# Optimization experiments

Hardware: AMD Instinct MI355X
Metric: run time of the kernel (lower is better)

The kernel has to match this reference:

```python
import jax, jax.numpy as jnp
import numpy as np

D_MODEL = 1024

def setup_inputs() -> dict:
    key = jax.random.key(0)
    ks = jax.random.split(key, 7)
    B, S, D = 4, 2048, D_MODEL
    scale = 1.0 / np.sqrt(D)
    x = jax.random.normal(ks[0], (B, S, D), dtype=jnp.float32)
    Wq = jax.random.normal(ks[1], (D, D), dtype=jnp.float32) * scale
    bq = jax.random.normal(ks[2], (D,), dtype=jnp.float32) * 0.02
    Wk = jax.random.normal(ks[3], (D, D), dtype=jnp.float32) * scale
    bk = jax.random.normal(ks[4], (D,), dtype=jnp.float32) * 0.02
    Wv = jax.random.normal(ks[5], (D, D), dtype=jnp.float32) * scale
    bv = jax.random.normal(ks[6], (D,), dtype=jnp.float32) * 0.02
    return {"x": x, "Wq": Wq, "bq": bq, "Wk": Wk, "bk": bk, "Wv": Wv, "bv": bv}

def reference(x, Wq, bq, Wk, bk, Wv, bv):
    # x: [B, S, D]
    B, S, D = x.shape
    q = jnp.einsum('bsd,de->bse', x, Wq) + bq
    k = jnp.einsum('bsd,de,->bse'.replace(',->', '->'), x, Wk) + bk
    v = jnp.einsum('bsd,de->bse', x, Wv) + bv
    # scores: [B, S, S], scaled by 1/sqrt(d_model) with additive causal mask
    scores = jnp.einsum('bqd,bkd->bqk', q, k) / jnp.sqrt(jnp.float32(D))
    causal = jnp.triu(jnp.full((S, S), -jnp.inf, dtype=scores.dtype), k=1)
    probs = jax.nn.softmax(scores + causal, axis=-1)
    return jnp.einsum('bqk,bkd->bqd', probs, v)
```

## Files before the change

### kernel.cpp

```cpp
#include <hip/hip_runtime.h>
#include <hip/hip_bf16.h>

#define S_LEN 2048
#define DM 1024
#define NB 4

typedef __attribute__((ext_vector_type(8))) short short8;
typedef __attribute__((ext_vector_type(4))) short short4v;
typedef __attribute__((ext_vector_type(4))) float floatx4;

__device__ inline short f2bf(float f) {
    union { float f; unsigned u; } v; v.f = f;
    unsigned r = 0x7fffu + ((v.u >> 16) & 1u);
    return (short)((v.u + r) >> 16);
}

__device__ inline void load16(const short* g, short* l) {
    __builtin_amdgcn_global_load_lds(
        (const __attribute__((address_space(1))) void*)g,
        (__attribute__((address_space(3))) void*)l,
        16, 0, 0);
}

__device__ inline void gemm_core128(const short* __restrict__ A,
                                    const short* __restrict__ Bt,
                                    int lda, int ldb, int kLen,
                                    int m0, int n0, floatx4 acc[4][4],
                                    short* As, short* Bs) {
    const int tid  = threadIdx.x;
    const int lane = tid & 63;
    const int wave = tid >> 6;
    const int wr   = (wave >> 1) * 64;
    const int wc   = (wave & 1) * 64;
    const int quad = lane >> 4;
    const int l16  = lane & 15;

    const int srow = tid >> 4;
    const int g    = (tid & 15) ^ srow;
    const short* gA0 = A  + (size_t)(m0 + srow) * lda + g * 8;
    const short* gB0 = Bt + (size_t)(n0 + srow) * ldb + g * 8;
    short* lA0 = &As[wave * 512];
    short* lB0 = &Bs[wave * 512];

    const short* fa[4]; const short* fb[4];
#pragma unroll
    for (int h = 0; h < 4; h++) {
        int sw = ((h * 4 + quad) ^ l16) * 8;
        fa[h] = &As[(wr + l16) * 128 + sw];
        fb[h] = &Bs[(wc + l16) * 128 + sw];
    }

    for (int k0 = 0; k0 < kLen; k0 += 128) {
#pragma unroll
        for (int c = 0; c < 8; c++) load16(gA0 + (size_t)c * 16 * lda, lA0 + c * 2048);
#pragma unroll
        for (int c = 0; c < 8; c++) load16(gB0 + (size_t)c * 16 * ldb, lB0 + c * 2048);
        gA0 += 128; gB0 += 128;
        __syncthreads();

#pragma unroll
        for (int h = 0; h < 4; h++) {
            short8 af[4], bf[4];
#pragma unroll
            for (int t = 0; t < 4; t++) af[t] = *(const short8*)(fa[h] + t * 2048);
#pragma unroll
            for (int t = 0; t < 4; t++) bf[t] = *(const short8*)(fb[h] + t * 2048);
#pragma unroll
            for (int mt = 0; mt < 4; mt++)
#pragma unroll
                for (int nt = 0; nt < 4; nt++)
                    acc[mt][nt] = __builtin_amdgcn_mfma_f32_16x16x32_bf16(
                        af[mt], bf[nt], acc[mt][nt], 0, 0, 0);
        }
        __syncthreads();
    }
}

__global__ void prep(const float* __restrict__ x,
                     const float* __restrict__ Wq, const float* __restrict__ Wk,
                     const float* __restrict__ Wv,
                     short* __restrict__ xb, short* __restrict__ Wt,
                     float* __restrict__ denom) {
    __shared__ float t[64][65];
    int bid = blockIdx.x, tid = threadIdx.x;
    if (bid < 768) {
        int w = bid >> 8, tl = bid & 255;
        const float* W = (w == 0) ? Wq : (w == 1) ? Wk : Wv;
        short* out = Wt + (size_t)w * DM * DM;
        int bx = (tl & 15) * 64;
        int by = (tl >> 4) * 64;
        int tx = tid & 63, ty = tid >> 6;
        for (int r = ty; r < 64; r += 4)
            t[r][tx] = W[(size_t)(by + r) * DM + bx + tx];
        __syncthreads();
        for (int r = ty; r < 64; r += 4)
            out[(size_t)(bx + r) * DM + by + tx] = f2bf(t[tx][r]);
    } else if (bid < 768 + 8192) {
        int i = (bid - 768) * 256 + tid;
        float4 v = ((const float4*)x)[i];
        short4v o;
        o.x = f2bf(v.x); o.y = f2bf(v.y); o.z = f2bf(v.z); o.w = f2bf(v.w);
        ((short4v*)xb)[i] = o;
    } else {
        int i = (bid - 8960) * 256 + tid;
        if (i < NB * S_LEN) denom[i] = 0.f;
    }
}

__global__ __launch_bounds__(256, 2)
void qkv_fused(const short* __restrict__ xb, const short* __restrict__ Wt,
               const float* __restrict__ bq, const float* __restrict__ bk,
               const float* __restrict__ bv,
               short* __restrict__ Qb, short* __restrict__ Kb,
               short* __restrict__ Vtb) {
    __shared__ short As[8192];
    __shared__ short Bs[3 * 8192];
    int n0 = blockIdx.x * 128;
    int m0 = blockIdx.y * 128;

    const int tid  = threadIdx.x;
    const int lane = tid & 63;
    const int wave = tid >> 6;
    const int wr   = (wave >> 1) * 64;
    const int wc   = (wave & 1) * 64;
    const int quad = lane >> 4;
    const int l16  = lane & 15;

    floatx4 acc[3][4][4];
#pragma unroll
    for (int w = 0; w < 3; w++)
#pragma unroll
        for (int i = 0; i < 4; i++)
#pragma unroll
            for (int j = 0; j < 4; j++) acc[w][i][j] = (floatx4){0.f, 0.f, 0.f, 0.f};

    const short* gA[4]; const short* gW[4];
    short* lA[4]; short* lB[4];
#pragma unroll
    for (int c = 0; c < 4; c++) {
        int idx = c * 256 + tid;
        int row = idx >> 3;
        int g = (idx & 7) ^ (row & 7);
        gA[c] = xb + (size_t)(m0 + row) * DM + g * 8;
        gW[c] = Wt + (size_t)(n0 + row) * DM + g * 8;
        int lbase = (c * 256 + wave * 64) * 8;
        lA[c] = &As[lbase];
        lB[c] = &Bs[lbase];
    }

    const short* fa[2]; const short* fb[2];
#pragma unroll
    for (int h = 0; h < 2; h++) {
        int sw = ((h * 4 + quad) ^ (l16 & 7)) * 8;
        fa[h] = &As[(wr + l16) * 64 + sw];
        fb[h] = &Bs[(wc + l16) * 64 + sw];
    }

    for (int k0 = 0; k0 < DM; k0 += 64) {
#pragma unroll
        for (int c = 0; c < 4; c++) load16(gA[c], lA[c]);
#pragma unroll
        for (int w = 0; w < 3; w++)
#pragma unroll
            for (int c = 0; c < 4; c++)
                load16(gW[c] + (size_t)w * DM * DM, lB[c] + w * 8192);
#pragma unroll
        for (int c = 0; c < 4; c++) { gA[c] += 64; gW[c] += 64; }
        __syncthreads();

#pragma unroll
        for (int h = 0; h < 2; h++) {
            short8 af[4];
#pragma unroll
            for (int t = 0; t < 4; t++) af[t] = *(const short8*)(fa[h] + t * 1024);
#pragma unroll
            for (int w = 0; w < 3; w++) {
                short8 bf[4];
#pragma unroll
                for (int t = 0; t < 4; t++)
                    bf[t] = *(const short8*)(fb[h] + w * 8192 + t * 1024);
#pragma unroll
                for (int mt = 0; mt < 4; mt++)
#pragma unroll
                    for (int nt = 0; nt < 4; nt++)
                        acc[w][mt][nt] = __builtin_amdgcn_mfma_f32_16x16x32_bf16(
                            af[mt], bf[nt], acc[w][mt][nt], 0, 0, 0);
            }
        }
        __syncthreads();
    }

#pragma unroll
    for (int w = 0; w < 2; w++) {
        short* out = w ? Kb : Qb;
        const float* bias = w ? bk : bq;
        float scale = w ? 1.0f : 0.03125f;
#pragma unroll
        for (int mt = 0; mt < 4; mt++)
#pragma unroll
            for (int nt = 0; nt < 4; nt++) {
                int col = n0 + wc + nt * 16 + l16;
                float bv_ = bias[col];
#pragma unroll
                for (int r = 0; r < 4; r++) {
                    int row = m0 + wr + mt * 16 + quad * 4 + r;
                    out[(size_t)row * DM + col] = f2bf((acc[w][mt][nt][r] + bv_) * scale);
                }
            }
    }

    {
        int b = m0 >> 11;
        int sbase = (m0 & 2047) + wr;
        float bvv[4];
#pragma unroll
        for (int nt = 0; nt < 4; nt++) bvv[nt] = bv[n0 + wc + nt * 16 + l16];
        short* buf = (wave & 1) ? Bs : As;
        short* vt = Vtb + ((size_t)b * DM + n0 + wc) * S_LEN;
#pragma unroll
        for (int p = 0; p < 2; p++) {
            __syncthreads();
            if ((wave >> 1) == p) {
#pragma unroll
                for (int mt = 0; mt < 4; mt++)
#pragma unroll
                    for (int nt = 0; nt < 4; nt++) {
                        int c = nt * 16 + l16;
                        short4v pk;
                        pk.x = f2bf(acc[2][mt][nt][0] + bvv[nt]);
                        pk.y = f2bf(acc[2][mt][nt][1] + bvv[nt]);
                        pk.z = f2bf(acc[2][mt][nt][2] + bvv[nt]);
                        pk.w = f2bf(acc[2][mt][nt][3] + bvv[nt]);
                        *(short4v*)&buf[c * 72 + mt * 16 + quad * 4] = pk;
                    }
                asm volatile("s_waitcnt lgkmcnt(0)" ::: "memory");
#pragma unroll
                for (int ps = 0; ps < 8; ps++) {
                    int dl = ps * 8 + (lane >> 3);
                    int sl = (lane & 7) * 8;
                    short8 row = *(short8*)&buf[dl * 72 + sl];
                    *(short8*)(vt + (size_t)dl * S_LEN + sbase + sl) = row;
                }
            }
        }
    }
}

__global__ __launch_bounds__(256, 2)
void score_gemm(const short* __restrict__ Qb, const short* __restrict__ Kb,
                short* __restrict__ P, float* __restrict__ denom) {
    __shared__ short As[16384];
    __shared__ short Bs[16384];
    int b = blockIdx.z;
    int xq = 135 - (int)blockIdx.x;
    int it = (int)((sqrtf(8.0f * xq + 1.0f) - 1.0f) * 0.5f);
    while ((it + 1) * (it + 2) / 2 <= xq) it++;
    while (it * (it + 1) / 2 > xq) it--;
    int jt = xq - it * (it + 1) / 2;
    int n0 = jt * 128, m0 = it * 128;
    const short* A  = Qb + (size_t)b * S_LEN * DM;
    const short* Bt = Kb + (size_t)b * S_LEN * DM;

    floatx4 acc[4][4];
#pragma unroll
    for (int i = 0; i < 4; i++)
#pragma unroll
        for (int j = 0; j < 4; j++) acc[i][j] = (floatx4){0.f, 0.f, 0.f, 0.f};

    gemm_core128(A, Bt, DM, DM, DM, m0, n0, acc, As, Bs);

    short* out = P + (size_t)b * S_LEN * S_LEN;
    float* dsum = denom + (size_t)b * S_LEN;
    const int lane = threadIdx.x & 63, wave = threadIdx.x >> 6;
    const int wr = (wave >> 1) * 64, wc = (wave & 1) * 64;
    const int quad = lane >> 4, l16 = lane & 15;
    const bool diag = (jt == it);
#pragma unroll
    for (int mt = 0; mt < 4; mt++) {
#pragma unroll
        for (int r = 0; r < 4; r++) {
            int row = m0 + wr + mt * 16 + quad * 4 + r;
            float psum = 0.f;
#pragma unroll
            for (int nt = 0; nt < 4; nt++) {
                int col = n0 + wc + nt * 16 + l16;
                float e = __expf(acc[mt][nt][r]);
                if (diag && col > row) e = 0.f;
                out[(size_t)row * S_LEN + col] = f2bf(e);
                psum += e;
            }
#pragma unroll
            for (int off = 8; off > 0; off >>= 1)
                psum += __shfl_down(psum, off, 16);
            if (l16 == 0) atomicAdd(&dsum[row], psum);
        }
    }
}

__global__ __launch_bounds__(256, 2)
void pv_gemm(const short* __restrict__ P, const short* __restrict__ Vtb,
             const float* __restrict__ denom, float* __restrict__ O) {
    __shared__ short As[16384];
    __shared__ short Bs[16384];
    int bid = blockIdx.x;
    int it = 15 - (bid >> 5);
    int n0 = ((bid >> 2) & 7) * 128;
    int b  = bid & 3;
    int m0 = it * 128;
    int kLen = (it + 1) * 128;
    const short* A  = P   + (size_t)b * S_LEN * S_LEN;
    const short* Bt = Vtb + (size_t)b * DM * S_LEN;

    floatx4 acc[4][4];
#pragma unroll
    for (int i = 0; i < 4; i++)
#pragma unroll
        for (int j = 0; j < 4; j++) acc[i][j] = (floatx4){0.f, 0.f, 0.f, 0.f};

    gemm_core128(A, Bt, S_LEN, S_LEN, kLen, m0, n0, acc, As, Bs);

    float* out = O + (size_t)b * S_LEN * DM;
    const float* dsum = denom + (size_t)b * S_LEN;
    const int lane = threadIdx.x & 63, wave = threadIdx.x >> 6;
    const int wr = (wave >> 1) * 64, wc = (wave & 1) * 64;
    const int quad = lane >> 4, l16 = lane & 15;
#pragma unroll
    for (int mt = 0; mt < 4; mt++) {
#pragma unroll
        for (int r = 0; r < 4; r++) {
            int row = m0 + wr + mt * 16 + quad * 4 + r;
            float inv = 1.0f / dsum[row];
#pragma unroll
            for (int nt = 0; nt < 4; nt++) {
                int col = n0 + wc + nt * 16 + l16;
                out[(size_t)row * DM + col] = acc[mt][nt][r] * inv;
            }
        }
    }
}

extern "C" void kernel_launch(void* const* d_in, const int* in_sizes, int n_in,
                              void* d_out, int out_size, void* d_ws, size_t ws_size,
                              hipStream_t stream) {
    const float* x  = (const float*)d_in[0];
    const float* Wq = (const float*)d_in[1];
    const float* bq = (const float*)d_in[2];
    const float* Wk = (const float*)d_in[3];
    const float* bk = (const float*)d_in[4];
    const float* Wv = (const float*)d_in[5];
    const float* bv = (const float*)d_in[6];
    float* out = (float*)d_out;

    char* ws = (char*)d_ws;
    const size_t MB = 1u << 20;
    short* xb    = (short*)(ws + 0);
    short* Wt    = (short*)(ws + 16 * MB);
    short* Qb    = (short*)(ws + 22 * MB);
    short* Kb    = (short*)(ws + 38 * MB);
    short* Vtb   = (short*)(ws + 54 * MB);
    short* P     = (short*)(ws + 70 * MB);
    float* denom = (float*)(ws + 102 * MB);

    prep<<<dim3(8992), dim3(256), 0, stream>>>(x, Wq, Wk, Wv, xb, Wt, denom);
    qkv_fused<<<dim3(8, 64), dim3(256), 0, stream>>>(xb, Wt, bq, bk, bv, Qb, Kb, Vtb);
    score_gemm<<<dim3(136, 1, NB), dim3(256), 0, stream>>>(Qb, Kb, P, denom);
    pv_gemm<<<dim3(512), dim3(256), 0, stream>>>(P, Vtb, denom, out);
}
```

Before: 220.9 us.

## Rewrite QKV projection as 8-wave 256x128 tiles with triple-buffered LDS pipeline

Replaces the 4-wave kernel, where each block computed Q, K and V together for a 128x128 tile, with a 512-thread kernel. Each block now computes one 256x128 output tile of the concatenated QKV weight matrix, and the block index is swizzled for L2 locality. Global-to-LDS loads run in a 3-stage ring buffer with explicit vmcnt waits, split barriers and setprio, so memory traffic overlaps MFMA work. The cost is 144KB of dynamic LDS, which limits how many blocks fit per CU, and hand-placed waitcnts that are fragile to get right.

```diff
diff --git a/kernel.cpp b/kernel.cpp
--- a/kernel.cpp
+++ b/kernel.cpp
@@ -107,16 +107,20 @@
     }
 }
 
-__global__ __launch_bounds__(256, 2)
-void qkv_fused(const short* __restrict__ xb, const short* __restrict__ Wt,
-               const float* __restrict__ bq, const float* __restrict__ bk,
-               const float* __restrict__ bv,
-               short* __restrict__ Qb, short* __restrict__ Kb,
-               short* __restrict__ Vtb) {
-    __shared__ short As[8192];
-    __shared__ short Bs[3 * 8192];
-    int n0 = blockIdx.x * 128;
-    int m0 = blockIdx.y * 128;
+__global__ __launch_bounds__(512, 2)
+void qkv8(const short* __restrict__ xb, const short* __restrict__ Wt,
+          const float* __restrict__ bq, const float* __restrict__ bk,
+          const float* __restrict__ bv,
+          short* __restrict__ Qb, short* __restrict__ Kb,
+          short* __restrict__ Vtb) {
+    extern __shared__ short lds[];
+
+    const int bid = blockIdx.x;
+    const int swz = (bid & 7) * 96 + (bid >> 3);
+    const int nt  = swz % 24;
+    const int mt  = swz / 24;
+    const int m0  = mt * 256;
+    const int n0  = nt * 128;
 
     const int tid  = threadIdx.x;
     const int lane = tid & 63;
@@ -126,122 +130,147 @@
     const int quad = lane >> 4;
     const int l16  = lane & 15;
 
-    floatx4 acc[3][4][4];
-#pragma unroll
-    for (int w = 0; w < 3; w++)
-#pragma unroll
-        for (int i = 0; i < 4; i++)
-#pragma unroll
-            for (int j = 0; j < 4; j++) acc[w][i][j] = (floatx4){0.f, 0.f, 0.f, 0.f};
-
-    const short* gA[4]; const short* gW[4];
-    short* lA[4]; short* lB[4];
+    floatx4 acc[4][4];
+#pragma unroll
+    for (int i = 0; i < 4; i++)
+#pragma unroll
+        for (int j = 0; j < 4; j++) acc[i][j] = (floatx4){0.f, 0.f, 0.f, 0.f};
+
+    const short* gA[4]; const short* gB[2];
 #pragma unroll
     for (int c = 0; c < 4; c++) {
-        int idx = c * 256 + tid;
+        int idx = c * 512 + tid;
         int row = idx >> 3;
         int g = (idx & 7) ^ (row & 7);
         gA[c] = xb + (size_t)(m0 + row) * DM + g * 8;
-        gW[c] = Wt + (size_t)(n0 + row) * DM + g * 8;
-        int lbase = (c * 256 + wave * 64) * 8;
-        lA[c] = &As[lbase];
-        lB[c] = &Bs[lbase];
-    }
-
-    const short* fa[2]; const short* fb[2];
-#pragma unroll
-    for (int h = 0; h < 2; h++) {
-        int sw = ((h * 4 + quad) ^ (l16 & 7)) * 8;
-        fa[h] = &As[(wr + l16) * 64 + sw];
-        fb[h] = &Bs[(wc + l16) * 64 + sw];
-    }
-
-    for (int k0 = 0; k0 < DM; k0 += 64) {
-#pragma unroll
-        for (int c = 0; c < 4; c++) load16(gA[c], lA[c]);
-#pragma unroll
-        for (int w = 0; w < 3; w++)
-#pragma unroll
-            for (int c = 0; c < 4; c++)
-                load16(gW[c] + (size_t)w * DM * DM, lB[c] + w * 8192);
-#pragma unroll
-        for (int c = 0; c < 4; c++) { gA[c] += 64; gW[c] += 64; }
-        __syncthreads();
-
-#pragma unroll
-        for (int h = 0; h < 2; h++) {
-            short8 af[4];
-#pragma unroll
-            for (int t = 0; t < 4; t++) af[t] = *(const short8*)(fa[h] + t * 1024);
-#pragma unroll
-            for (int w = 0; w < 3; w++) {
-                short8 bf[4];
-#pragma unroll
-                for (int t = 0; t < 4; t++)
-                    bf[t] = *(const short8*)(fb[h] + w * 8192 + t * 1024);
-#pragma unroll
-                for (int mt = 0; mt < 4; mt++)
-#pragma unroll
-                    for (int nt = 0; nt < 4; nt++)
-                        acc[w][mt][nt] = __builtin_amdgcn_mfma_f32_16x16x32_bf16(
-                            af[mt], bf[nt], acc[w][mt][nt], 0, 0, 0);
-            }
-        }
-        __syncthreads();
-    }
-
-#pragma unroll
-    for (int w = 0; w < 2; w++) {
+    }
+#pragma unroll
+    for (int c = 0; c < 2; c++) {
+        int idx = c * 512 + tid;
+        int row = idx >> 3;
+        int g = (idx & 7) ^ (row & 7);
+        gB[c] = Wt + (size_t)(n0 + row) * DM + g * 8;
+    }
+    const int ldsAoff = wave * 512;
+    const int ldsBoff = 16384 + wave * 512;
+
+#pragma unroll
+    for (int c = 0; c < 4; c++) load16(gA[c], lds + ldsAoff + c * 4096);
+#pragma unroll
+    for (int c = 0; c < 2; c++) load16(gB[c], lds + ldsBoff + c * 4096);
+#pragma unroll
+    for (int c = 0; c < 4; c++) load16(gA[c] + 64, lds + 24576 + ldsAoff + c * 4096);
+#pragma unroll
+    for (int c = 0; c < 2; c++) load16(gB[c] + 64, lds + 24576 + ldsBoff + c * 4096);
+    asm volatile("s_waitcnt vmcnt(6)" ::: "memory");
+    __builtin_amdgcn_s_barrier();
+    __builtin_amdgcn_sched_barrier(0);
+
+    for (int k = 0; k < 16; k++) {
+        const int cur = k % 3;
+        const int nx2 = (k + 2) % 3;
+        const short* Ab = lds + cur * 24576;
+        const short* Bb = Ab + 16384;
+        short* sA = lds + nx2 * 24576 + ldsAoff;
+        short* sB = lds + nx2 * 24576 + ldsBoff;
+        const int koff = (k + 2) * 64;
+
+#pragma unroll
+        for (int kk = 0; kk < 2; kk++) {
+            short8 af[4], bf[4];
+#pragma unroll
+            for (int mf = 0; mf < 4; mf++) {
+                int row = wr + mf * 16 + l16;
+                int sw = ((kk * 4 + quad) ^ (l16 & 7)) * 8;
+                af[mf] = *(const short8*)(Ab + row * 64 + sw);
+            }
+#pragma unroll
+            for (int nf = 0; nf < 4; nf++) {
+                int row = wc + nf * 16 + l16;
+                int sw = ((kk * 4 + quad) ^ (l16 & 7)) * 8;
+                bf[nf] = *(const short8*)(Bb + row * 64 + sw);
+            }
+            if (k <= 13) {
+                if (kk == 0) {
+                    load16(gA[0] + koff, sA);
+                    load16(gA[1] + koff, sA + 4096);
+                    load16(gB[0] + koff, sB);
+                    load16(gB[1] + koff, sB + 4096);
+                } else {
+                    load16(gA[2] + koff, sA + 8192);
+                    load16(gA[3] + koff, sA + 12288);
+                }
+            }
+            asm volatile("s_waitcnt lgkmcnt(0)" ::: "memory");
+            __builtin_amdgcn_sched_barrier(0);
+            __builtin_amdgcn_s_setprio(1);
+#pragma unroll
+            for (int mf = 0; mf < 4; mf++)
+#pragma unroll
+                for (int nf = 0; nf < 4; nf++)
+                    acc[mf][nf] = __builtin_amdgcn_mfma_f32_16x16x32_bf16(
+                        af[mf], bf[nf], acc[mf][nf], 0, 0, 0);
+            __builtin_amdgcn_s_setprio(0);
+            if (kk == 0) {
+                __builtin_amdgcn_s_barrier();
+                __builtin_amdgcn_sched_barrier(0);
+            }
+        }
+        if (k <= 13) {
+            asm volatile("s_waitcnt vmcnt(6)" ::: "memory");
+        } else if (k == 14) {
+            asm volatile("s_waitcnt vmcnt(0)" ::: "memory");
+        }
+        __builtin_amdgcn_s_barrier();
+        __builtin_amdgcn_sched_barrier(0);
+    }
+
+    const int w  = n0 >> 10;
+    const int cw = n0 & 1023;
+
+    if (w < 2) {
         short* out = w ? Kb : Qb;
         const float* bias = w ? bk : bq;
         float scale = w ? 1.0f : 0.03125f;
 #pragma unroll
-        for (int mt = 0; mt < 4; mt++)
-#pragma unroll
-            for (int nt = 0; nt < 4; nt++) {
-                int col = n0 + wc + nt * 16 + l16;
+        for (int mf = 0; mf < 4; mf++)
+#pragma unroll
+            for (int nf = 0; nf < 4; nf++) {
+                int col = cw + wc + nf * 16 + l16;
                 float bv_ = bias[col];
 #pragma unroll
                 for (int r = 0; r < 4; r++) {
-                    int row = m0 + wr + mt * 16 + quad * 4 + r;
-                    out[(size_t)row * DM + col] = f2bf((acc[w][mt][nt][r] + bv_) * scale);
+                    int row = m0 + wr + mf * 16 + quad * 4 + r;
+                    out[(size_t)row * DM + col] = f2bf((acc[mf][nf][r] + bv_) * scale);
                 }
             }
-    }
-
-    {
+    } else {
         int b = m0 >> 11;
         int sbase = (m0 & 2047) + wr;
         float bvv[4];
 #pragma unroll
-        for (int nt = 0; nt < 4; nt++) bvv[nt] = bv[n0 + wc + nt * 16 + l16];
-        short* buf = (wave & 1) ? Bs : As;
-        short* vt = Vtb + ((size_t)b * DM + n0 + wc) * S_LEN;
-#pragma unroll
-        for (int p = 0; p < 2; p++) {
-            __syncthreads();
-            if ((wave >> 1) == p) {
-#pragma unroll
-                for (int mt = 0; mt < 4; mt++)
-#pragma unroll
-                    for (int nt = 0; nt < 4; nt++) {
-                        int c = nt * 16 + l16;
-                        short4v pk;
-                        pk.x = f2bf(acc[2][mt][nt][0] + bvv[nt]);
-                        pk.y = f2bf(acc[2][mt][nt][1] + bvv[nt]);
-                        pk.z = f2bf(acc[2][mt][nt][2] + bvv[nt]);
-                        pk.w = f2bf(acc[2][mt][nt][3] + bvv[nt]);
-                        *(short4v*)&buf[c * 72 + mt * 16 + quad * 4] = pk;
-                    }
-                asm volatile("s_waitcnt lgkmcnt(0)" ::: "memory");
-#pragma unroll
-                for (int ps = 0; ps < 8; ps++) {
-                    int dl = ps * 8 + (lane >> 3);
-                    int sl = (lane & 7) * 8;
-                    short8 row = *(short8*)&buf[dl * 72 + sl];
-                    *(short8*)(vt + (size_t)dl * S_LEN + sbase + sl) = row;
-                }
-            }
+        for (int nf = 0; nf < 4; nf++) bvv[nf] = bv[cw + wc + nf * 16 + l16];
+        short* buf = lds + wave * 4608;
+        short* vt = Vtb + ((size_t)b * DM + cw + wc) * S_LEN;
+#pragma unroll
+        for (int mf = 0; mf < 4; mf++)
+#pragma unroll
+            for (int nf = 0; nf < 4; nf++) {
+                int c = nf * 16 + l16;
+                short4v pk;
+                pk.x = f2bf(acc[mf][nf][0] + bvv[nf]);
+                pk.y = f2bf(acc[mf][nf][1] + bvv[nf]);
+                pk.z = f2bf(acc[mf][nf][2] + bvv[nf]);
+                pk.w = f2bf(acc[mf][nf][3] + bvv[nf]);
+                *(short4v*)&buf[c * 72 + mf * 16 + quad * 4] = pk;
+            }
+        asm volatile("s_waitcnt lgkmcnt(0)" ::: "memory");
+#pragma unroll
+        for (int ps = 0; ps < 8; ps++) {
+            int dl = ps * 8 + (lane >> 3);
+            int sl = (lane & 7) * 8;
+            short8 row = *(short8*)&buf[dl * 72 + sl];
+            *(short8*)(vt + (size_t)dl * S_LEN + sbase + sl) = row;
         }
     }
 }
@@ -361,8 +390,15 @@
     short* P     = (short*)(ws + 70 * MB);
     float* denom = (float*)(ws + 102 * MB);
 
+    static bool attr_set = false;
+    if (!attr_set) {
+        hipFuncSetAttribute(reinterpret_cast<const void*>(qkv8),
+                            hipFuncAttributeMaxDynamicSharedMemorySize, 147456);
+        attr_set = true;
+    }
+
     prep<<<dim3(8992), dim3(256), 0, stream>>>(x, Wq, Wk, Wv, xb, Wt, denom);
-    qkv_fused<<<dim3(8, 64), dim3(256), 0, stream>>>(xb, Wt, bq, bk, bv, Qb, Kb, Vtb);
+    qkv8<<<dim3(768), dim3(512), 147456, stream>>>(xb, Wt, bq, bk, bv, Qb, Kb, Vtb);
     score_gemm<<<dim3(136, 1, NB), dim3(256), 0, stream>>>(Qb, Kb, P, denom);
     pv_gemm<<<dim3(512), dim3(256), 0, stream>>>(P, Vtb, denom, out);
 }
```

After: 234.4 us. 1.06x slower.
